# Performance work log

Measured on AMD Instinct MI355X. Metric: run time of the kernel, lower is better.

The kernel has to match this reference:

```python
import jax, jax.numpy as jnp
import numpy as np

N_HEAD = 8

def _l2norm(x, eps=1e-12):
    # F.normalize(p=2, dim=-1): x / max(||x||_2, eps)
    return x / jnp.maximum(jnp.linalg.norm(x, axis=-1, keepdims=True), eps)

def setup_inputs() -> dict:
    key = jax.random.key(0)
    ks = jax.random.split(key, 9)
    B, L, E = 2, 2048, 512
    s = 0.02
    return {
        "query": jax.random.normal(ks[0], (B, L, E), dtype=jnp.float32),
        "Wq": s * jax.random.normal(ks[1], (E, E), dtype=jnp.float32),
        "bq": jnp.zeros((E,), dtype=jnp.float32),
        "Wk": s * jax.random.normal(ks[2], (E, E), dtype=jnp.float32),
        "bk": jnp.zeros((E,), dtype=jnp.float32),
        "Wv": s * jax.random.normal(ks[3], (E, E), dtype=jnp.float32),
        "bv": jnp.zeros((E,), dtype=jnp.float32),
        "Wo": s * jax.random.normal(ks[4], (E, E), dtype=jnp.float32),
        "bo": jnp.zeros((E,), dtype=jnp.float32),
    }

def reference(query, Wq, bq, Wk, bk, Wv, bv, Wo, bo):
    B, L, E = query.shape
    H = N_HEAD
    hd = E // H
    # Faithful to torch: .view(tgt_len, bsz, E) is a RESHAPE, not a transpose.
    x = query.reshape(L, B, E)
    q = jax.nn.relu(x @ Wq.T + bq)
    k = jax.nn.relu(x @ Wk.T + bk)
    v = x @ Wv.T + bv
    q = _l2norm(q)
    k = _l2norm(k)
    # (L, B, E) -> (L, B*H, hd) -> (B*H, L, hd)
    q_ = q.reshape(L, B * H, hd).transpose(1, 0, 2)
    k_ = k.reshape(L, B * H, hd).transpose(1, 0, 2)
    v_ = v.reshape(L, B * H, hd).transpose(1, 0, 2)
    # Causal linear attention: cumulative outer-product of k,v then contract with q.
    kv = jnp.einsum('nld,nlm->nldm', k_, v_)      # [B*H, L, hd, hd]
    kv_cum = jnp.cumsum(kv, axis=1)
    out = jnp.einsum('nld,nldm->nlm', q_, kv_cum)  # [B*H, L, hd]
    out = out.transpose(1, 0, 2).reshape(L, B, E)
    out = out @ Wo.T + bo
    return out.reshape(B, L, E)
```

## Files before the change

### kernel.cpp

```cpp
#include <hip/hip_runtime.h>
#include <hip/hip_bf16.h>

typedef __attribute__((ext_vector_type(8))) short short8;
typedef __attribute__((ext_vector_type(4))) float f32x4;
using bf16 = __hip_bfloat16;

__device__ __forceinline__ unsigned short f2bf(float f) {
    unsigned u = __float_as_uint(f);
    u += 0x7fff + ((u >> 16) & 1);
    return (unsigned short)(u >> 16);
}
__device__ __forceinline__ float bf2f(unsigned short s) {
    return __uint_as_float(((unsigned)s) << 16);
}
__device__ __forceinline__ void cvt8_store(unsigned short* dst, float4 a, float4 b) {
    ushort4 u0, u1;
    u0.x = f2bf(a.x); u0.y = f2bf(a.y); u0.z = f2bf(a.z); u0.w = f2bf(a.w);
    u1.x = f2bf(b.x); u1.y = f2bf(b.y); u1.z = f2bf(b.z); u1.w = f2bf(b.w);
    *(ushort4*)dst = u0;
    *(ushort4*)(dst + 4) = u1;
}

__global__ __launch_bounds__(256) void qkv_gemm_kernel(
    const float* __restrict__ X,
    const float* __restrict__ W0, const float* __restrict__ W1, const float* __restrict__ W2,
    const float* __restrict__ b0, const float* __restrict__ b1, const float* __restrict__ b2,
    bf16* __restrict__ O0, bf16* __restrict__ O1, bf16* __restrict__ O2,
    float* __restrict__ ssq)
{
    __shared__ __align__(16) unsigned short smem[8192];
    unsigned short* As = smem;
    unsigned short* Bs = smem + 2560;
    int z = blockIdx.z;
    const float* W = (z == 0) ? W0 : ((z == 1) ? W1 : W2);
    const float* bias = (z == 0) ? b0 : ((z == 1) ? b1 : b2);
    unsigned short* Out = (unsigned short*)((z == 0) ? O0 : ((z == 1) ? O1 : O2));

    int m0 = blockIdx.x * 64;
    int n0 = blockIdx.y * 128;
    int tid = threadIdx.x;
    int lane = tid & 63;
    int wave = tid >> 6;
    int wm = (wave >> 1) * 32;
    int wn = (wave & 1) * 64;
    int fr = lane & 15, q = lane >> 4;

    f32x4 zero4 = {0.f, 0.f, 0.f, 0.f};
    f32x4 acc[2][4];
    #pragma unroll
    for (int t = 0; t < 2; ++t)
        #pragma unroll
        for (int u = 0; u < 4; ++u) acc[t][u] = zero4;

    int srow = tid >> 2;
    int skk  = (tid & 3) * 8;

    for (int k0 = 0; k0 < 512; k0 += 32) {
        __syncthreads();
        {
            const float* ap = X + (size_t)(m0 + srow) * 512 + k0 + skk;
            cvt8_store(&As[srow * 40 + skk], *(const float4*)ap, *(const float4*)(ap + 4));
            #pragma unroll
            for (int rep = 0; rep < 2; ++rep) {
                int r = rep * 64 + srow;
                const float* bp = W + (size_t)(n0 + r) * 512 + k0 + skk;
                cvt8_store(&Bs[r * 40 + skk], *(const float4*)bp, *(const float4*)(bp + 4));
            }
        }
        __syncthreads();
        short8 af[2], bfr[4];
        #pragma unroll
        for (int t = 0; t < 2; ++t) af[t] = *(const short8*)&As[(wm + t * 16 + fr) * 40 + q * 8];
        #pragma unroll
        for (int u = 0; u < 4; ++u) bfr[u] = *(const short8*)&Bs[(wn + u * 16 + fr) * 40 + q * 8];
        #pragma unroll
        for (int t = 0; t < 2; ++t)
            #pragma unroll
            for (int u = 0; u < 4; ++u)
                acc[t][u] = __builtin_amdgcn_mfma_f32_16x16x32_bf16(af[t], bfr[u], acc[t][u], 0, 0, 0);
    }

    bool relu = (z < 2);
    int rb = q * 4;
    #pragma unroll
    for (int t = 0; t < 2; ++t)
        #pragma unroll
        for (int u = 0; u < 4; ++u) {
            float bv = bias[n0 + wn + u * 16 + fr];
            #pragma unroll
            for (int r = 0; r < 4; ++r) {
                float v = acc[t][u][r] + bv;
                if (relu) v = fmaxf(v, 0.f);
                acc[t][u][r] = v;
            }
        }
    if (relu) {
        #pragma unroll
        for (int t = 0; t < 2; ++t)
            #pragma unroll
            for (int r = 0; r < 4; ++r) {
                float s = 0.f;
                #pragma unroll
                for (int u = 0; u < 4; ++u) s += acc[t][u][r] * acc[t][u][r];
                #pragma unroll
                for (int off = 1; off < 16; off <<= 1) s += __shfl_xor(s, off, 64);
                if (fr == 0) atomicAdd(&ssq[z * 4096 + m0 + wm + t * 16 + rb + r], s);
            }
    }
    __syncthreads();
    #pragma unroll
    for (int t = 0; t < 2; ++t)
        #pragma unroll
        for (int u = 0; u < 4; ++u)
            #pragma unroll
            for (int r = 0; r < 4; ++r)
                smem[(wm + t * 16 + rb + r) * 128 + wn + u * 16 + fr] = f2bf(acc[t][u][r]);
    __syncthreads();
    #pragma unroll
    for (int rep = 0; rep < 4; ++rep) {
        int idx8 = rep * 256 + tid;
        int row = idx8 >> 4, col8 = (idx8 & 15) * 8;
        *(uint4*)(Out + (size_t)(m0 + row) * 512 + n0 + col8) = *(const uint4*)&smem[row * 128 + col8];
    }
}

__global__ __launch_bounds__(256) void chunk_kv_kernel(
    const bf16* __restrict__ Kb, const bf16* __restrict__ Vb,
    const float* __restrict__ ssq, float* __restrict__ ScT, bf16* __restrict__ Vt_g)
{
    int n = blockIdx.x >> 4, c = blockIdx.x & 15;
    int b = n >> 3, h = n & 7;
    __shared__ float Ks[64 * 64];
    __shared__ float Vs[64 * 64];
    const unsigned short* Kg = (const unsigned short*)Kb;
    const unsigned short* Vg = (const unsigned short*)Vb;
    int tid = threadIdx.x;
    int td = tid >> 4, tm = tid & 15;
    int d0 = td * 4, m0 = tm * 4;
    int vm = tid & 63, vj0 = (tid >> 6) * 16;
    float acc[4][4] = {};
    for (int half = 0; half < 2; ++half) {
        __syncthreads();
        #pragma unroll
        for (int rep = 0; rep < 4; ++rep) {
            int idx = rep * 1024 + tid * 4;
            int j = idx >> 6, d = idx & 63;
            int grow = (c * 128 + half * 64 + j) * 2 + b;
            ushort4 ku = *(const ushort4*)&Kg[(size_t)grow * 512 + h * 64 + d];
            ushort4 vu = *(const ushort4*)&Vg[(size_t)grow * 512 + h * 64 + d];
            float rk = 1.f / fmaxf(sqrtf(ssq[4096 + grow]), 1e-12f);
            *(float4*)&Ks[j * 64 + d] = make_float4(bf2f(ku.x), bf2f(ku.y), bf2f(ku.z), bf2f(ku.w));
            *(float4*)&Vs[j * 64 + d] = make_float4(bf2f(vu.x) * rk, bf2f(vu.y) * rk,
                                                    bf2f(vu.z) * rk, bf2f(vu.w) * rk);
        }
        __syncthreads();
        for (int j = 0; j < 64; ++j) {
            float4 kv = *(const float4*)&Ks[j * 64 + d0];
            float4 vv = *(const float4*)&Vs[j * 64 + m0];
            acc[0][0] += kv.x*vv.x; acc[0][1] += kv.x*vv.y; acc[0][2] += kv.x*vv.z; acc[0][3] += kv.x*vv.w;
            acc[1][0] += kv.y*vv.x; acc[1][1] += kv.y*vv.y; acc[1][2] += kv.y*vv.z; acc[1][3] += kv.y*vv.w;
            acc[2][0] += kv.z*vv.x; acc[2][1] += kv.z*vv.y; acc[2][2] += kv.z*vv.z; acc[2][3] += kv.z*vv.w;
            acc[3][0] += kv.w*vv.x; acc[3][1] += kv.w*vv.y; acc[3][2] += kv.w*vv.z; acc[3][3] += kv.w*vv.w;
        }
        unsigned short tmp[16];
        #pragma unroll
        for (int i = 0; i < 16; ++i) tmp[i] = f2bf(Vs[(vj0 + i) * 64 + vm]);
        size_t vtoff = (size_t)n * 131072 + (size_t)vm * 2048 + c * 128 + half * 64 + vj0;
        *(uint4*)((unsigned short*)Vt_g + vtoff)     = *(uint4*)&tmp[0];
        *(uint4*)((unsigned short*)Vt_g + vtoff + 8) = *(uint4*)&tmp[8];
    }
    float* outp = ScT + (size_t)blockIdx.x * 4096;
    #pragma unroll
    for (int j2 = 0; j2 < 4; ++j2) {
        float4 o4 = make_float4(acc[0][j2], acc[1][j2], acc[2][j2], acc[3][j2]);
        *(float4*)&outp[(m0 + j2) * 64 + d0] = o4;
    }
}

__global__ __launch_bounds__(256) void prefix_kernel(const float* __restrict__ ScT, bf16* __restrict__ SpT)
{
    int n = blockIdx.x >> 4;
    int idx = ((blockIdx.x & 15) << 8) + threadIdx.x;
    size_t base = (size_t)n * 65536 + idx;
    unsigned short* sp = (unsigned short*)SpT;
    float run = 0.f;
    #pragma unroll
    for (int c = 0; c < 16; ++c) {
        size_t off = base + (size_t)c * 4096;
        sp[off] = f2bf(run);
        run += ScT[off];
    }
}

__global__ __launch_bounds__(256) void attn_kernel(
    const bf16* __restrict__ Qb, const bf16* __restrict__ Kb,
    const bf16* __restrict__ Vt_g, const bf16* __restrict__ SpT_g,
    const float* __restrict__ ssq, bf16* __restrict__ AOb)
{
    int n = blockIdx.x >> 4, c = blockIdx.x & 15;
    int b = n >> 3, h = n & 7;
    __shared__ unsigned short Qs[128 * 72];
    __shared__ unsigned short Ks[128 * 72];
    __shared__ unsigned short Vt[64 * 136];
    __shared__ unsigned short Ps[4 * 32 * 40];
    int tid = threadIdx.x;
    int lane = tid & 63;
    int w = tid >> 6;
    int fr = lane & 15, q = lane >> 4;

    const unsigned short* Qg = (const unsigned short*)Qb;
    const unsigned short* Kg = (const unsigned short*)Kb;
    const unsigned short* Vg = (const unsigned short*)Vt_g;

    #pragma unroll
    for (int rep = 0; rep < 4; ++rep) {
        int idx = rep * 256 + tid;
        int l = idx >> 3, dc = (idx & 7) * 8;
        size_t goff = (size_t)((c * 128 + l) * 2 + b) * 512 + h * 64 + dc;
        *(uint4*)&Qs[l * 72 + dc] = *(const uint4*)(Qg + goff);
        *(uint4*)&Ks[l * 72 + dc] = *(const uint4*)(Kg + goff);
    }
    #pragma unroll
    for (int rep = 0; rep < 4; ++rep) {
        int idx = rep * 256 + tid;
        int m = idx >> 4, jc = (idx & 15) * 8;
        *(uint4*)&Vt[m * 136 + jc] =
            *(const uint4*)(Vg + (size_t)n * 131072 + (size_t)m * 2048 + c * 128 + jc);
    }
    __syncthreads();

    short8 qf[2][2];
    #pragma unroll
    for (int lt = 0; lt < 2; ++lt)
        #pragma unroll
        for (int kh = 0; kh < 2; ++kh)
            qf[lt][kh] = *(const short8*)&Qs[(w * 32 + lt * 16 + fr) * 72 + kh * 32 + q * 8];

    f32x4 zero4 = {0.f, 0.f, 0.f, 0.f};
    f32x4 oacc[2][4];
    #pragma unroll
    for (int lt = 0; lt < 2; ++lt)
        #pragma unroll
        for (int mt = 0; mt < 4; ++mt) oacc[lt][mt] = zero4;

    const unsigned short* spg = (const unsigned short*)SpT_g + (size_t)blockIdx.x * 4096;
    #pragma unroll
    for (int mt = 0; mt < 4; ++mt) {
        #pragma unroll
        for (int kh = 0; kh < 2; ++kh) {
            short8 sf = *(const short8*)&spg[(mt * 16 + fr) * 64 + kh * 32 + q * 8];
            oacc[0][mt] = __builtin_amdgcn_mfma_f32_16x16x32_bf16(qf[0][kh], sf, oacc[0][mt], 0, 0, 0);
            oacc[1][mt] = __builtin_amdgcn_mfma_f32_16x16x32_bf16(qf[1][kh], sf, oacc[1][mt], 0, 0, 0);
        }
    }

    unsigned short* myPs = &Ps[w * 1280];
    int rbase = q * 4;
    for (int jt = 0; jt <= w; ++jt) {
        f32x4 pacc[2][2];
        pacc[0][0] = zero4; pacc[0][1] = zero4; pacc[1][0] = zero4; pacc[1][1] = zero4;
        #pragma unroll
        for (int jt16 = 0; jt16 < 2; ++jt16) {
            #pragma unroll
            for (int kh = 0; kh < 2; ++kh) {
                short8 kf = *(const short8*)&Ks[(jt * 32 + jt16 * 16 + fr) * 72 + kh * 32 + q * 8];
                pacc[0][jt16] = __builtin_amdgcn_mfma_f32_16x16x32_bf16(qf[0][kh], kf, pacc[0][jt16], 0, 0, 0);
                pacc[1][jt16] = __builtin_amdgcn_mfma_f32_16x16x32_bf16(qf[1][kh], kf, pacc[1][jt16], 0, 0, 0);
            }
        }
        bool diag = (jt == w);
        #pragma unroll
        for (int lt = 0; lt < 2; ++lt)
            #pragma unroll
            for (int jt16 = 0; jt16 < 2; ++jt16)
                #pragma unroll
                for (int r = 0; r < 4; ++r) {
                    int ll = lt * 16 + rbase + r;
                    int jl = jt16 * 16 + fr;
                    float pv = pacc[lt][jt16][r];
                    if (diag && jl > ll) pv = 0.f;
                    myPs[ll * 40 + jl] = f2bf(pv);
                }
        short8 pf0 = *(const short8*)&myPs[fr * 40 + q * 8];
        short8 pf1 = *(const short8*)&myPs[(16 + fr) * 40 + q * 8];
        #pragma unroll
        for (int mt = 0; mt < 4; ++mt) {
            short8 vf = *(const short8*)&Vt[(mt * 16 + fr) * 136 + jt * 32 + q * 8];
            oacc[0][mt] = __builtin_amdgcn_mfma_f32_16x16x32_bf16(pf0, vf, oacc[0][mt], 0, 0, 0);
            oacc[1][mt] = __builtin_amdgcn_mfma_f32_16x16x32_bf16(pf1, vf, oacc[1][mt], 0, 0, 0);
        }
    }

    float rqv[2][4];
    #pragma unroll
    for (int lt = 0; lt < 2; ++lt)
        #pragma unroll
        for (int r = 0; r < 4; ++r) {
            int flat = (c * 128 + w * 32 + lt * 16 + rbase + r) * 2 + b;
            rqv[lt][r] = 1.f / fmaxf(sqrtf(ssq[flat]), 1e-12f);
        }
    __syncthreads();
    #pragma unroll
    for (int lt = 0; lt < 2; ++lt)
        #pragma unroll
        for (int mt = 0; mt < 4; ++mt)
            #pragma unroll
            for (int r = 0; r < 4; ++r)
                Qs[(w * 32 + lt * 16 + rbase + r) * 64 + mt * 16 + fr] = f2bf(oacc[lt][mt][r] * rqv[lt][r]);
    __syncthreads();
    #pragma unroll
    for (int rep = 0; rep < 4; ++rep) {
        int idx8 = rep * 256 + tid;
        int l = idx8 >> 3, m8 = (idx8 & 7) * 8;
        *(uint4*)((unsigned short*)AOb + (size_t)((c * 128 + l) * 2 + b) * 512 + h * 64 + m8) =
            *(const uint4*)&Qs[l * 64 + m8];
    }
}

__global__ __launch_bounds__(256) void oproj_kernel(
    const bf16* __restrict__ A, const float* __restrict__ W,
    const float* __restrict__ bias, float* __restrict__ Out)
{
    __shared__ __align__(16) unsigned short smem[8192];
    unsigned short* As = smem;
    unsigned short* Bs = smem + 2560;
    const unsigned short* Ag = (const unsigned short*)A;
    int m0 = blockIdx.x * 64;
    int n0 = blockIdx.y * 64;
    int tid = threadIdx.x;
    int lane = tid & 63;
    int wave = tid >> 6;
    int fr = lane & 15, q = lane >> 4;
    int wm = (wave >> 1) * 32;
    int wn = (wave & 1) * 32;

    f32x4 zero4 = {0.f, 0.f, 0.f, 0.f};
    f32x4 acc[2][2];
    acc[0][0] = zero4; acc[0][1] = zero4; acc[1][0] = zero4; acc[1][1] = zero4;

    int srow = tid >> 2;
    int skk  = (tid & 3) * 8;

    for (int k0 = 0; k0 < 512; k0 += 32) {
        __syncthreads();
        *(uint4*)&As[srow * 40 + skk] = *(const uint4*)(Ag + (size_t)(m0 + srow) * 512 + k0 + skk);
        {
            const float* bp = W + (size_t)(n0 + srow) * 512 + k0 + skk;
            cvt8_store(&Bs[srow * 40 + skk], *(const float4*)bp, *(const float4*)(bp + 4));
        }
        __syncthreads();
        short8 af[2], bf[2];
        #pragma unroll
        for (int t = 0; t < 2; ++t) af[t] = *(const short8*)&As[(wm + t * 16 + fr) * 40 + q * 8];
        #pragma unroll
        for (int u = 0; u < 2; ++u) bf[u] = *(const short8*)&Bs[(wn + u * 16 + fr) * 40 + q * 8];
        #pragma unroll
        for (int t = 0; t < 2; ++t)
            #pragma unroll
            for (int u = 0; u < 2; ++u)
                acc[t][u] = __builtin_amdgcn_mfma_f32_16x16x32_bf16(af[t], bf[u], acc[t][u], 0, 0, 0);
    }

    int rb = q * 4;
    float* Cf = (float*)smem;
    __syncthreads();
    #pragma unroll
    for (int t = 0; t < 2; ++t)
        #pragma unroll
        for (int u = 0; u < 2; ++u) {
            float bv = bias[n0 + wn + u * 16 + fr];
            #pragma unroll
            for (int r = 0; r < 4; ++r)
                Cf[(wm + t * 16 + rb + r) * 64 + wn + u * 16 + fr] = acc[t][u][r] + bv;
        }
    __syncthreads();
    #pragma unroll
    for (int rep = 0; rep < 4; ++rep) {
        int idx = rep * 256 + tid;
        int row = idx >> 4, c4 = (idx & 15) * 4;
        *(float4*)(Out + (size_t)(m0 + row) * 512 + n0 + c4) = *(const float4*)&Cf[row * 64 + c4];
    }
}

extern "C" void kernel_launch(void* const* d_in, const int* in_sizes, int n_in,
                              void* d_out, int out_size, void* d_ws, size_t ws_size,
                              hipStream_t stream)
{
    (void)in_sizes; (void)n_in; (void)out_size; (void)ws_size;
    const float* x  = (const float*)d_in[0];
    const float* Wq = (const float*)d_in[1];
    const float* bq = (const float*)d_in[2];
    const float* Wk = (const float*)d_in[3];
    const float* bk = (const float*)d_in[4];
    const float* Wv = (const float*)d_in[5];
    const float* bv = (const float*)d_in[6];
    const float* Wo = (const float*)d_in[7];
    const float* bo = (const float*)d_in[8];
    float* out = (float*)d_out;

    float* ssq = (float*)d_ws;
    bf16* Qb  = (bf16*)(ssq + 8192);
    bf16* Kb  = Qb + 2097152;
    bf16* Vb  = Kb + 2097152;
    bf16* Vt  = Vb + 2097152;
    bf16* AOb = Vt + 2097152;
    bf16* SpT = AOb + 2097152;
    float* ScT = (float*)(SpT + 1048576);

    hipMemsetAsync(ssq, 0, 8192 * sizeof(float), stream);
    qkv_gemm_kernel<<<dim3(64, 4, 3), 256, 0, stream>>>(x, Wq, Wk, Wv, bq, bk, bv, Qb, Kb, Vb, ssq);
    chunk_kv_kernel<<<dim3(256), 256, 0, stream>>>(Kb, Vb, ssq, ScT, Vt);
    prefix_kernel<<<dim3(256), 256, 0, stream>>>(ScT, SpT);
    attn_kernel<<<dim3(256), 256, 0, stream>>>(Qb, Kb, Vt, SpT, ssq, AOb);
    oproj_kernel<<<dim3(64, 8), 256, 0, stream>>>(AOb, Wo, bo, out);
}
```

Baseline: 128.6 us.

## Pre-pack inputs and weights to bf16 and load GEMM tiles via global_load_lds

Adds a pack kernel that converts X and all four weight matrices from fp32 to bf16 in a k-sliced, MFMA-friendly tiled layout, and folds the ssq zeroing into it instead of a memset. The QKV and output-projection GEMMs then load tiles straight into LDS with global_load_lds, with no per-element conversion in the inner loop. The output projection also widens its N tile to 128, matching the QKV kernel's blocking. The cost is an extra launch and an extra round trip of X and the weights through memory, and weights are re-packed on every call.

```diff
diff --git a/kernel.cpp b/kernel.cpp
--- a/kernel.cpp
+++ b/kernel.cpp
@@ -13,37 +13,77 @@
 __device__ __forceinline__ float bf2f(unsigned short s) {
     return __uint_as_float(((unsigned)s) << 16);
 }
-__device__ __forceinline__ void cvt8_store(unsigned short* dst, float4 a, float4 b) {
-    ushort4 u0, u1;
-    u0.x = f2bf(a.x); u0.y = f2bf(a.y); u0.z = f2bf(a.z); u0.w = f2bf(a.w);
-    u1.x = f2bf(b.x); u1.y = f2bf(b.y); u1.z = f2bf(b.z); u1.w = f2bf(b.w);
-    *(ushort4*)dst = u0;
-    *(ushort4*)(dst + 4) = u1;
+__device__ __forceinline__ void gl_lds16(const unsigned short* g, unsigned short* l) {
+    __builtin_amdgcn_global_load_lds(
+        (const __attribute__((address_space(1))) unsigned int*)g,
+        (__attribute__((address_space(3))) unsigned int*)l, 16, 0, 0);
+}
+
+
+__global__ __launch_bounds__(256) void pack_kernel(
+    const float* __restrict__ X, const float* __restrict__ Wq, const float* __restrict__ Wk,
+    const float* __restrict__ Wv, const float* __restrict__ Wo,
+    bf16* __restrict__ Xp, bf16* __restrict__ Wqp, bf16* __restrict__ Wkp,
+    bf16* __restrict__ Wvp, bf16* __restrict__ Wop, float* __restrict__ ssq)
+{
+    __shared__ __align__(16) unsigned short sm[4096];
+    int id = blockIdx.x;
+    int tid = threadIdx.x;
+    if (id < 8) {
+        int zi = id * 1024 + tid * 4;
+        *(float4*)&ssq[zi] = make_float4(0.f, 0.f, 0.f, 0.f);
+    }
+    const float* src; unsigned short* dst; int g, sc;
+    if (id < 512) { src = X; dst = (unsigned short*)Xp; g = id >> 3; sc = id & 7; }
+    else {
+        int t = id - 512; int wsel = t >> 6; int u = t & 63;
+        g = u >> 3; sc = u & 7;
+        src = (wsel == 0) ? Wq : ((wsel == 1) ? Wk : ((wsel == 2) ? Wv : Wo));
+        dst = (unsigned short*)((wsel == 0) ? Wqp : ((wsel == 1) ? Wkp : ((wsel == 2) ? Wvp : Wop)));
+    }
+    int r = tid >> 2, kq = tid & 3;
+    const float* sp = src + (size_t)(g * 64 + r) * 512 + sc * 64 + kq * 16;
+    #pragma unroll
+    for (int i = 0; i < 4; ++i) {
+        float4 v = *(const float4*)(sp + i * 4);
+        int kk = kq * 16 + i * 4;
+        int sl = kk >> 3, el = kk & 7;
+        ushort4 u4;
+        u4.x = f2bf(v.x); u4.y = f2bf(v.y); u4.z = f2bf(v.z); u4.w = f2bf(v.w);
+        *(ushort4*)&sm[(sl * 64 + r) * 8 + el] = u4;
+    }
+    __syncthreads();
+    unsigned short* dp = dst + (size_t)g * 32768 + sc * 4096;
+    *(uint4*)(dp + tid * 16)     = *(const uint4*)&sm[tid * 16];
+    *(uint4*)(dp + tid * 16 + 8) = *(const uint4*)&sm[tid * 16 + 8];
 }
 
 __global__ __launch_bounds__(256) void qkv_gemm_kernel(
-    const float* __restrict__ X,
-    const float* __restrict__ W0, const float* __restrict__ W1, const float* __restrict__ W2,
+    const bf16* __restrict__ Xp,
+    const bf16* __restrict__ W0p, const bf16* __restrict__ W1p, const bf16* __restrict__ W2p,
     const float* __restrict__ b0, const float* __restrict__ b1, const float* __restrict__ b2,
     bf16* __restrict__ O0, bf16* __restrict__ O1, bf16* __restrict__ O2,
     float* __restrict__ ssq)
 {
     __shared__ __align__(16) unsigned short smem[8192];
     unsigned short* As = smem;
-    unsigned short* Bs = smem + 2560;
+    unsigned short* Bs = smem + 2048;
     int z = blockIdx.z;
-    const float* W = (z == 0) ? W0 : ((z == 1) ? W1 : W2);
+    const unsigned short* Wg = (const unsigned short*)((z == 0) ? W0p : ((z == 1) ? W1p : W2p));
     const float* bias = (z == 0) ? b0 : ((z == 1) ? b1 : b2);
     unsigned short* Out = (unsigned short*)((z == 0) ? O0 : ((z == 1) ? O1 : O2));
-
-    int m0 = blockIdx.x * 64;
+    const unsigned short* Ag = (const unsigned short*)Xp;
+
+    int g  = blockIdx.x;
+    int gB = blockIdx.y * 2;
+    int m0 = g * 64;
     int n0 = blockIdx.y * 128;
     int tid = threadIdx.x;
     int lane = tid & 63;
-    int wave = tid >> 6;
-    int wm = (wave >> 1) * 32;
-    int wn = (wave & 1) * 64;
-    int fr = lane & 15, q = lane >> 4;
+    int w = tid >> 6;
+    int wm = (w >> 1) * 32;
+    int wn = (w & 1) * 64;
+    int fr = lane & 15, qf = lane >> 4;
 
     f32x4 zero4 = {0.f, 0.f, 0.f, 0.f};
     f32x4 acc[2][4];
@@ -52,27 +92,18 @@
         #pragma unroll
         for (int u = 0; u < 4; ++u) acc[t][u] = zero4;
 
-    int srow = tid >> 2;
-    int skk  = (tid & 3) * 8;
-
-    for (int k0 = 0; k0 < 512; k0 += 32) {
-        __syncthreads();
-        {
-            const float* ap = X + (size_t)(m0 + srow) * 512 + k0 + skk;
-            cvt8_store(&As[srow * 40 + skk], *(const float4*)ap, *(const float4*)(ap + 4));
-            #pragma unroll
-            for (int rep = 0; rep < 2; ++rep) {
-                int r = rep * 64 + srow;
-                const float* bp = W + (size_t)(n0 + r) * 512 + k0 + skk;
-                cvt8_store(&Bs[r * 40 + skk], *(const float4*)bp, *(const float4*)(bp + 4));
-            }
-        }
+    for (int kw = 0; kw < 16; ++kw) {
+        int s0 = kw * 4;
+        __syncthreads();
+        gl_lds16(Ag + ((size_t)(g * 64 + s0 + w) * 64 + lane) * 8, As + w * 512);
+        gl_lds16(Wg + ((size_t)(gB * 64 + s0 + w) * 64 + lane) * 8, Bs + w * 1024);
+        gl_lds16(Wg + ((size_t)((gB + 1) * 64 + s0 + w) * 64 + lane) * 8, Bs + w * 1024 + 512);
         __syncthreads();
         short8 af[2], bfr[4];
         #pragma unroll
-        for (int t = 0; t < 2; ++t) af[t] = *(const short8*)&As[(wm + t * 16 + fr) * 40 + q * 8];
-        #pragma unroll
-        for (int u = 0; u < 4; ++u) bfr[u] = *(const short8*)&Bs[(wn + u * 16 + fr) * 40 + q * 8];
+        for (int t = 0; t < 2; ++t) af[t] = *(const short8*)&As[(qf * 64 + wm + t * 16 + fr) * 8];
+        #pragma unroll
+        for (int u = 0; u < 4; ++u) bfr[u] = *(const short8*)&Bs[(qf * 128 + wn + u * 16 + fr) * 8];
         #pragma unroll
         for (int t = 0; t < 2; ++t)
             #pragma unroll
@@ -81,7 +112,7 @@
     }
 
     bool relu = (z < 2);
-    int rb = q * 4;
+    int rb = qf * 4;
     #pragma unroll
     for (int t = 0; t < 2; ++t)
         #pragma unroll
@@ -318,67 +349,70 @@
 }
 
 __global__ __launch_bounds__(256) void oproj_kernel(
-    const bf16* __restrict__ A, const float* __restrict__ W,
+    const bf16* __restrict__ A, const bf16* __restrict__ Wop,
     const float* __restrict__ bias, float* __restrict__ Out)
 {
-    __shared__ __align__(16) unsigned short smem[8192];
+    __shared__ __align__(16) unsigned short smem[16384];
     unsigned short* As = smem;
     unsigned short* Bs = smem + 2560;
     const unsigned short* Ag = (const unsigned short*)A;
+    const unsigned short* Wg = (const unsigned short*)Wop;
     int m0 = blockIdx.x * 64;
-    int n0 = blockIdx.y * 64;
+    int gB = blockIdx.y * 2;
+    int n0 = blockIdx.y * 128;
     int tid = threadIdx.x;
     int lane = tid & 63;
-    int wave = tid >> 6;
-    int fr = lane & 15, q = lane >> 4;
-    int wm = (wave >> 1) * 32;
-    int wn = (wave & 1) * 32;
-
-    f32x4 zero4 = {0.f, 0.f, 0.f, 0.f};
-    f32x4 acc[2][2];
-    acc[0][0] = zero4; acc[0][1] = zero4; acc[1][0] = zero4; acc[1][1] = zero4;
-
+    int w = tid >> 6;
+    int fr = lane & 15, qf = lane >> 4;
+    int wm = (w >> 1) * 32;
+    int wn = (w & 1) * 64;
     int srow = tid >> 2;
     int skk  = (tid & 3) * 8;
 
-    for (int k0 = 0; k0 < 512; k0 += 32) {
+    f32x4 zero4 = {0.f, 0.f, 0.f, 0.f};
+    f32x4 acc[2][4];
+    #pragma unroll
+    for (int t = 0; t < 2; ++t)
+        #pragma unroll
+        for (int u = 0; u < 4; ++u) acc[t][u] = zero4;
+
+    for (int kw = 0; kw < 16; ++kw) {
+        int k0 = kw * 32, s0 = kw * 4;
         __syncthreads();
         *(uint4*)&As[srow * 40 + skk] = *(const uint4*)(Ag + (size_t)(m0 + srow) * 512 + k0 + skk);
-        {
-            const float* bp = W + (size_t)(n0 + srow) * 512 + k0 + skk;
-            cvt8_store(&Bs[srow * 40 + skk], *(const float4*)bp, *(const float4*)(bp + 4));
-        }
-        __syncthreads();
-        short8 af[2], bf[2];
-        #pragma unroll
-        for (int t = 0; t < 2; ++t) af[t] = *(const short8*)&As[(wm + t * 16 + fr) * 40 + q * 8];
-        #pragma unroll
-        for (int u = 0; u < 2; ++u) bf[u] = *(const short8*)&Bs[(wn + u * 16 + fr) * 40 + q * 8];
+        gl_lds16(Wg + ((size_t)(gB * 64 + s0 + w) * 64 + lane) * 8, Bs + w * 1024);
+        gl_lds16(Wg + ((size_t)((gB + 1) * 64 + s0 + w) * 64 + lane) * 8, Bs + w * 1024 + 512);
+        __syncthreads();
+        short8 af[2], bfr[4];
+        #pragma unroll
+        for (int t = 0; t < 2; ++t) af[t] = *(const short8*)&As[(wm + t * 16 + fr) * 40 + qf * 8];
+        #pragma unroll
+        for (int u = 0; u < 4; ++u) bfr[u] = *(const short8*)&Bs[(qf * 128 + wn + u * 16 + fr) * 8];
         #pragma unroll
         for (int t = 0; t < 2; ++t)
             #pragma unroll
-            for (int u = 0; u < 2; ++u)
-                acc[t][u] = __builtin_amdgcn_mfma_f32_16x16x32_bf16(af[t], bf[u], acc[t][u], 0, 0, 0);
-    }
-
-    int rb = q * 4;
+            for (int u = 0; u < 4; ++u)
+                acc[t][u] = __builtin_amdgcn_mfma_f32_16x16x32_bf16(af[t], bfr[u], acc[t][u], 0, 0, 0);
+    }
+
+    int rb = qf * 4;
     float* Cf = (float*)smem;
     __syncthreads();
     #pragma unroll
     for (int t = 0; t < 2; ++t)
         #pragma unroll
-        for (int u = 0; u < 2; ++u) {
+        for (int u = 0; u < 4; ++u) {
             float bv = bias[n0 + wn + u * 16 + fr];
             #pragma unroll
             for (int r = 0; r < 4; ++r)
-                Cf[(wm + t * 16 + rb + r) * 64 + wn + u * 16 + fr] = acc[t][u][r] + bv;
-        }
-    __syncthreads();
-    #pragma unroll
-    for (int rep = 0; rep < 4; ++rep) {
+                Cf[(wm + t * 16 + rb + r) * 128 + wn + u * 16 + fr] = acc[t][u][r] + bv;
+        }
+    __syncthreads();
+    #pragma unroll
+    for (int rep = 0; rep < 8; ++rep) {
         int idx = rep * 256 + tid;
-        int row = idx >> 4, c4 = (idx & 15) * 4;
-        *(float4*)(Out + (size_t)(m0 + row) * 512 + n0 + c4) = *(const float4*)&Cf[row * 64 + c4];
+        int row = idx >> 5, c4 = (idx & 31) * 4;
+        *(float4*)(Out + (size_t)(m0 + row) * 512 + n0 + c4) = *(const float4*)&Cf[row * 128 + c4];
     }
 }
 
@@ -399,7 +433,12 @@
     float* out = (float*)d_out;
 
     float* ssq = (float*)d_ws;
-    bf16* Qb  = (bf16*)(ssq + 8192);
+    bf16* Xp  = (bf16*)(ssq + 8192);
+    bf16* Wqp = Xp + 2097152;
+    bf16* Wkp = Wqp + 262144;
+    bf16* Wvp = Wkp + 262144;
+    bf16* Wop = Wvp + 262144;
+    bf16* Qb  = Wop + 262144;
     bf16* Kb  = Qb + 2097152;
     bf16* Vb  = Kb + 2097152;
     bf16* Vt  = Vb + 2097152;
@@ -407,10 +446,10 @@
     bf16* SpT = AOb + 2097152;
     float* ScT = (float*)(SpT + 1048576);
 
-    hipMemsetAsync(ssq, 0, 8192 * sizeof(float), stream);
-    qkv_gemm_kernel<<<dim3(64, 4, 3), 256, 0, stream>>>(x, Wq, Wk, Wv, bq, bk, bv, Qb, Kb, Vb, ssq);
+    pack_kernel<<<768, 256, 0, stream>>>(x, Wq, Wk, Wv, Wo, Xp, Wqp, Wkp, Wvp, Wop, ssq);
+    qkv_gemm_kernel<<<dim3(64, 4, 3), 256, 0, stream>>>(Xp, Wqp, Wkp, Wvp, bq, bk, bv, Qb, Kb, Vb, ssq);
     chunk_kv_kernel<<<dim3(256), 256, 0, stream>>>(Kb, Vb, ssq, ScT, Vt);
     prefix_kernel<<<dim3(256), 256, 0, stream>>>(ScT, SpT);
     attn_kernel<<<dim3(256), 256, 0, stream>>>(Qb, Kb, Vt, SpT, ssq, AOb);
-    oproj_kernel<<<dim3(64, 8), 256, 0, stream>>>(AOb, Wo, bo, out);
-}
+    oproj_kernel<<<dim3(64, 4), 256, 0, stream>>>(AOb, Wop, bo, out);
+}
```

Result: faster. 123.6 us (-3.9%).
